# Optimization experiments

Hardware: AMD Instinct MI355X
Metric: run time of the kernel (lower is better)

The kernel has to match this reference:

```python
import jax, jax.numpy as jnp
import numpy as np

H = 16  # num heads


def setup_inputs() -> dict:
    key = jax.random.key(0)
    ks = jax.random.split(key, 12)
    B, S, D = 2, 2048, 1024
    f = lambda k, shape: jax.random.normal(k, shape, dtype=jnp.float32) * 0.02
    return {
        "Q": jax.random.normal(ks[0], (B, S, D), dtype=jnp.float32),
        "K": jax.random.normal(ks[1], (B, S, D), dtype=jnp.float32),
        "V": jax.random.normal(ks[2], (B, S, D), dtype=jnp.float32),
        "mask": jax.random.randint(ks[3], (B, S, S), 0, 2, dtype=jnp.int32),
        "Wq": f(ks[4], (D, D)), "bq": f(ks[5], (D,)),
        "Wk": f(ks[6], (D, D)), "bk": f(ks[7], (D,)),
        "Wv": f(ks[8], (D, D)), "bv": f(ks[9], (D,)),
        "Wo": f(ks[10], (D, D)), "bo": f(ks[11], (D,)),
    }


def mha(Q, K, V, mask, Wq, bq, Wk, bk, Wv, bv, Wo, bo):
    B, S, D = Q.shape
    d_k = D // H
    # torch Linear: x @ W.T + b
    q = (Q @ Wq.T + bq).reshape(B, S, H, d_k).transpose(0, 2, 1, 3)  # [B,H,S,dk]
    k = (K @ Wk.T + bk).reshape(B, S, H, d_k).transpose(0, 2, 1, 3)
    v = (V @ Wv.T + bv).reshape(B, S, H, d_k).transpose(0, 2, 1, 3)
    scores = jnp.einsum('bhqd,bhkd->bhqk', q, k) / jnp.sqrt(jnp.float32(d_k))
    # faithful to torch: mask.repeat(H,1,1) tiles batch-major along dim0 of [B*H,S,S]
    m = jnp.tile(mask, (H, 1, 1)).reshape(B, H, S, S)
    scores = jnp.where(m == 0, jnp.float32(-1e9), scores)
    attn = jax.nn.softmax(scores, axis=-1)                 # [B,H,S,S]
    ctx = jnp.einsum('bhqk,bhkd->bhqd', attn, v)           # [B,H,S,dk]
    ctx = ctx.transpose(0, 2, 1, 3).reshape(B, S, D)
    out = ctx @ Wo.T + bo
    return out, attn


def reference(Q, K, V, mask, Wq, bq, Wk, bk, Wv, bv, Wo, bo):
    return mha(Q, K, V, mask, Wq, bq, Wk, bk, Wv, bv, Wo, bo)
```

## Files before the change

kernel.cpp:

```cpp
#include <hip/hip_runtime.h>
#include <stdint.h>


typedef __attribute__((ext_vector_type(8))) short bf16x8;
typedef __attribute__((ext_vector_type(4))) float f32x4;
typedef unsigned long long u64;

#define MFMA16(a, b, c) __builtin_amdgcn_mfma_f32_16x16x32_bf16((a), (b), (c), 0, 0, 0)

#define GLDS16(g, l)                                                   \
  __builtin_amdgcn_global_load_lds(                                    \
      (const __attribute__((address_space(1))) unsigned int*)(g),      \
      (__attribute__((address_space(3))) unsigned int*)(l), 16, 0, 0)

__device__ __forceinline__ float bf2f(short s) {
  union { float f; unsigned u; } x;
  x.u = ((unsigned)(unsigned short)s) << 16;
  return x.f;
}
__device__ __forceinline__ short f2bf(float f) {
  union { float f; unsigned u; } x;
  x.f = f;
  unsigned r = x.u + 0x7fffu + ((x.u >> 16) & 1u);
  return (short)(r >> 16);
}
__device__ __forceinline__ unsigned cvtpk2(float lo, float hi) {
  unsigned r;
  asm("v_cvt_pk_bf16_f32 %0, %1, %2" : "=v"(r) : "v"(lo), "v"(hi));
  return r;
}
__device__ __forceinline__ bf16x8 pack8(float4 a, float4 b) {
  union { unsigned u[4]; bf16x8 v; } x;
  x.u[0] = cvtpk2(a.x, a.y);
  x.u[1] = cvtpk2(a.z, a.w);
  x.u[2] = cvtpk2(b.x, b.y);
  x.u[3] = cvtpk2(b.z, b.w);
  return x.v;
}

__global__ __launch_bounds__(256) void sentinel_fill(float* __restrict__ out,
                                                     float v, int n) {
  int i = blockIdx.x * 256 + threadIdx.x;
  if (i < n) out[i] = v;
}

__global__ __launch_bounds__(256) void pack_mask(const int* __restrict__ m,
                                                 u64* __restrict__ p) {
  long idx = (long)blockIdx.x * 256 + threadIdx.x;
  u64 b = __ballot(m[idx] != 0);
  if ((threadIdx.x & 63) == 0) p[idx >> 6] = b;
}

struct QkvPtrs {
  const float *A0, *A1, *A2;
  const float *W0, *W1, *W2;
  const float *c0, *c1, *c2;
  short *o0, *o1, *o2;
};
__global__ __launch_bounds__(256) void gemm_qkv(QkvPtrs p) {
  __shared__ short As[128 * 32];
  __shared__ short Bs[128 * 32];
  const int z = blockIdx.z;
  const float* Af = z == 0 ? p.A0 : (z == 1 ? p.A1 : p.A2);
  const float* W = z == 0 ? p.W0 : (z == 1 ? p.W1 : p.W2);
  const float* bias = z == 0 ? p.c0 : (z == 1 ? p.c1 : p.c2);
  short* outs = z == 0 ? p.o0 : (z == 1 ? p.o1 : p.o2);

  const int tid = threadIdx.x;
  const int lane = tid & 63;
  const int wid = tid >> 6;
  const int wr = wid >> 1, wc = wid & 1;
  const int m0 = blockIdx.x * 128;
  const int n0 = blockIdx.y * 128;

  const int srow = tid >> 1;
  const int scol = (tid & 1) << 4;
  const long aoff = (long)(m0 + srow) * 1024 + scol;
  const float* Wg = W + (long)(n0 + srow) * 1024 + scol;
  short* sA = As + srow * 32 + scol;
  short* sB = Bs + srow * 32 + scol;

  f32x4 acc[4][4] = {};
  const int fr = lane & 15;
  const int fc = (lane >> 4) << 3;

  for (int k0 = 0; k0 < 1024; k0 += 32) {
    __syncthreads();
    float4 x0 = *(const float4*)(Af + aoff + k0);
    float4 x1 = *(const float4*)(Af + aoff + k0 + 4);
    float4 x2 = *(const float4*)(Af + aoff + k0 + 8);
    float4 x3 = *(const float4*)(Af + aoff + k0 + 12);
    float4 w0 = *(const float4*)(Wg + k0);
    float4 w1 = *(const float4*)(Wg + k0 + 4);
    float4 w2 = *(const float4*)(Wg + k0 + 8);
    float4 w3 = *(const float4*)(Wg + k0 + 12);
    *(bf16x8*)sA = pack8(x0, x1);
    *(bf16x8*)(sA + 8) = pack8(x2, x3);
    *(bf16x8*)sB = pack8(w0, w1);
    *(bf16x8*)(sB + 8) = pack8(w2, w3);
    __syncthreads();
    bf16x8 a[4], b[4];
#pragma unroll
    for (int i = 0; i < 4; ++i)
      a[i] = *(const bf16x8*)&As[(wr * 64 + i * 16 + fr) * 32 + fc];
#pragma unroll
    for (int i = 0; i < 4; ++i)
      b[i] = *(const bf16x8*)&Bs[(wc * 64 + i * 16 + fr) * 32 + fc];
#pragma unroll
    for (int i = 0; i < 4; ++i)
#pragma unroll
      for (int j = 0; j < 4; ++j)
        acc[i][j] = MFMA16(a[i], b[j], acc[i][j]);
  }

#pragma unroll
  for (int i = 0; i < 4; ++i) {
    const int row0 = m0 + wr * 64 + i * 16 + (lane >> 4) * 4;
#pragma unroll
    for (int j = 0; j < 4; ++j) {
      const int col = n0 + wc * 64 + j * 16 + fr;
      const float bv = bias[col];
      const int h = col >> 6, dd = col & 63;
      if (z != 2) {
#pragma unroll
        for (int r = 0; r < 4; ++r) {
          const int m = row0 + r;
          float val = acc[i][j][r] + bv;
          if (z == 0) val *= 0.125f;
          const long o = (((long)(m >> 11) * 16 + h) * 2048 + (m & 2047)) * 64 + dd;
          outs[o] = f2bf(val);
        }
      } else {
        const long o = (((long)(row0 >> 11) * 16 + h) * 64 + dd) * 2048 + (row0 & 2047);
        union { unsigned short us[4]; uint2 v; } pk;
#pragma unroll
        for (int r = 0; r < 4; ++r) pk.us[r] = (unsigned short)f2bf(acc[i][j][r] + bv);
        *(uint2*)&outs[o] = pk.v;
      }
    }
  }
}

__global__ __launch_bounds__(256) void gemm_out(const short* __restrict__ Ab,
                                                const float* __restrict__ W,
                                                const float* __restrict__ bias,
                                                float* __restrict__ outf) {
  __shared__ short As[128 * 32];
  __shared__ short Bs[128 * 32];
  const int tid = threadIdx.x;
  const int lane = tid & 63;
  const int wid = tid >> 6;
  const int wr = wid >> 1, wc = wid & 1;
  const int m0 = blockIdx.x * 128;
  const int n0 = blockIdx.y * 128;

  const int srow = tid >> 1;
  const int scol = (tid & 1) << 4;
  const long aoff = (long)(m0 + srow) * 1024 + scol;
  const float* Wg = W + (long)(n0 + srow) * 1024 + scol;
  short* sA = As + srow * 32 + scol;
  short* sB = Bs + srow * 32 + scol;

  f32x4 acc[4][4] = {};
  const int fr = lane & 15;
  const int fc = (lane >> 4) << 3;

  for (int k0 = 0; k0 < 1024; k0 += 32) {
    __syncthreads();
    bf16x8 va0 = *(const bf16x8*)(Ab + aoff + k0);
    bf16x8 va1 = *(const bf16x8*)(Ab + aoff + k0 + 8);
    float4 w0 = *(const float4*)(Wg + k0);
    float4 w1 = *(const float4*)(Wg + k0 + 4);
    float4 w2 = *(const float4*)(Wg + k0 + 8);
    float4 w3 = *(const float4*)(Wg + k0 + 12);
    *(bf16x8*)sA = va0;
    *(bf16x8*)(sA + 8) = va1;
    *(bf16x8*)sB = pack8(w0, w1);
    *(bf16x8*)(sB + 8) = pack8(w2, w3);
    __syncthreads();
    bf16x8 a[4], b[4];
#pragma unroll
    for (int i = 0; i < 4; ++i)
      a[i] = *(const bf16x8*)&As[(wr * 64 + i * 16 + fr) * 32 + fc];
#pragma unroll
    for (int i = 0; i < 4; ++i)
      b[i] = *(const bf16x8*)&Bs[(wc * 64 + i * 16 + fr) * 32 + fc];
#pragma unroll
    for (int i = 0; i < 4; ++i)
#pragma unroll
      for (int j = 0; j < 4; ++j)
        acc[i][j] = MFMA16(a[i], b[j], acc[i][j]);
  }

#pragma unroll
  for (int i = 0; i < 4; ++i) {
    const int row0 = m0 + wr * 64 + i * 16 + (lane >> 4) * 4;
#pragma unroll
    for (int j = 0; j < 4; ++j) {
      const int col = n0 + wc * 64 + j * 16 + fr;
      const float bv = bias[col];
#pragma unroll
      for (int r = 0; r < 4; ++r)
        outf[(long)(row0 + r) * 1024 + col] = acc[i][j][r] + bv;
    }
  }
}

__global__ __launch_bounds__(256) void attn_fused(
    const short* __restrict__ qw, const short* __restrict__ kw,
    const short* __restrict__ vtw, const u64* __restrict__ pm,
    float* __restrict__ attn, short* __restrict__ ctx) {
  __shared__ short Ks[2][4096];
  __shared__ short Vs[2][4096];
  __shared__ short P[4][1024];
  const int tid = threadIdx.x;
  const int lane = tid & 63;
  const int wid = tid >> 6;
  const int bh = blockIdx.x;
  const int mb = bh & 1;
  const int q0 = blockIdx.y * 64 + wid * 16;
  const int fr = lane & 15;
  const int fg = lane >> 4;
  short* Pw = P[wid];

  bf16x8 aq[2];
  {
    const short* qb = qw + ((long)bh * 2048 + q0 + fr) * 64 + fg * 8;
    aq[0] = *(const bf16x8*)qb;
    aq[1] = *(const bf16x8*)(qb + 32);
  }

  const u64* mbase = pm + ((long)mb * 2048 + q0) * 32;
  const short* kbase = kw + (long)bh * 2048 * 64;
  const short* vbase = vtw + (long)bh * 64 * 2048;
  const long arow = (long)bh * 2048 + q0;

  const int sidx0 = tid;
  const int sidx1 = 256 + tid;
  const int sr0 = sidx0 >> 3, ss0 = (sidx0 ^ sr0) & 7;
  const int sr1 = sidx1 >> 3, ss1 = (sidx1 ^ sr1) & 7;
  short* ldst0 = &Ks[0][0] + (long)(wid * 64) * 8;
  short* ldst1 = &Ks[0][0] + (long)(256 + wid * 64) * 8;
  const long kofs = (long)(&Vs[0][0] - &Ks[0][0]);

#define STAGE_K(buf, kt)                                              \
  {                                                                   \
    const short* s_ = kbase + (long)((kt) * 64) * 64;                 \
    GLDS16(s_ + sr0 * 64 + ss0 * 8, ldst0 + (buf) * 4096);            \
    GLDS16(s_ + sr1 * 64 + ss1 * 8, ldst1 + (buf) * 4096);            \
  }
#define STAGE_V(buf, kt)                                              \
  {                                                                   \
    const short* s_ = vbase + (kt) * 64;                              \
    GLDS16(s_ + (long)sr0 * 2048 + ss0 * 8, ldst0 + kofs + (buf) * 4096); \
    GLDS16(s_ + (long)sr1 * 2048 + ss1 * 8, ldst1 + kofs + (buf) * 4096); \
  }
#define SWZ(row, slot) (((row) << 6) + ((((slot) ^ ((row) & 7))) << 3))
#define PADDR(row, col) \
  (((row) << 6) + (((((col) >> 3) ^ ((row) & 7))) << 3) + ((col) & 7))
#define WRITEBACK(kt)                                                 \
  {                                                                   \
    _Pragma("unroll") for (int c = 0; c < 4; ++c) {                   \
      const int idx = c * 64 + lane;                                  \
      const int row = idx >> 4;                                       \
      const int col = (idx & 15) * 4;                                 \
      union { uint2 w; short s[4]; } v4;                              \
      v4.w = *(const uint2*)&Pw[PADDR(row, col)];                     \
      float4 f;                                                       \
      f.x = bf2f(v4.s[0]); f.y = bf2f(v4.s[1]);                       \
      f.z = bf2f(v4.s[2]); f.w = bf2f(v4.s[3]);                       \
      *(float4*)&attn[(arow + row) * 2048 + (kt) * 64 + col] = f;     \
    }                                                                 \
  }
#define WAITBAR(N)                                                    \
  {                                                                   \
    asm volatile("s_waitcnt vmcnt(" #N ")" ::: "memory");             \
    __builtin_amdgcn_sched_barrier(0);                                \
    __builtin_amdgcn_s_barrier();                                     \
    __builtin_amdgcn_sched_barrier(0);                                \
  }

  float rs = 0.f;
  STAGE_K(0, 0);
  u64 mrow = mbase[fr * 32 + 0];
  WAITBAR(1)
  int cur = 0;
  for (int kt = 0; kt < 32; ++kt) {
    u64 mrow_next = 0;
    if (kt < 31) {
      STAGE_K(cur ^ 1, kt + 1);
      mrow_next = mbase[fr * 32 + kt + 1];
    }
#pragma unroll
    for (int ni = 0; ni < 4; ++ni) {
      const int R = ni * 16 + fr;
      bf16x8 b0 = *(const bf16x8*)&Ks[cur][SWZ(R, fg)];
      bf16x8 b1 = *(const bf16x8*)&Ks[cur][SWZ(R, 4 + fg)];
      const int kb0 = ni * 16 + fg * 4;
      const unsigned m4 = (unsigned)(mrow >> kb0) & 0xFu;
      f32x4 s = {0.f, 0.f, 0.f, 0.f};
      s = MFMA16(b0, aq[0], s);
      s = MFMA16(b1, aq[1], s);
#pragma unroll
      for (int r = 0; r < 4; ++r)
        if ((m4 >> r) & 1u) rs += __expf(s[r]);
    }
    if (kt < 31) {
      WAITBAR(1)
      cur ^= 1;
      mrow = mrow_next;
    }
  }
  float il;
  {
    float v = rs;
    v += __shfl_xor(v, 16);
    v += __shfl_xor(v, 32);
    il = 1.0f / v;
  }
  __builtin_amdgcn_s_barrier();

  f32x4 cacc[4] = {};
  STAGE_K(0, 0);
  STAGE_V(0, 0);
  mrow = mbase[fr * 32 + 0];
  WAITBAR(1)
  cur = 0;
  for (int kt = 0; kt < 32; ++kt) {
    u64 mrow_next = 0;
    if (kt < 31) {
      STAGE_K(cur ^ 1, kt + 1);
      STAGE_V(cur ^ 1, kt + 1);
      mrow_next = mbase[fr * 32 + kt + 1];
    }

#pragma unroll
    for (int ni = 0; ni < 4; ++ni) {
      const int R = ni * 16 + fr;
      bf16x8 b0 = *(const bf16x8*)&Ks[cur][SWZ(R, fg)];
      bf16x8 b1 = *(const bf16x8*)&Ks[cur][SWZ(R, 4 + fg)];
      const int kb0 = ni * 16 + fg * 4;
      const unsigned m4 = (unsigned)(mrow >> kb0) & 0xFu;
      f32x4 s = {0.f, 0.f, 0.f, 0.f};
      s = MFMA16(b0, aq[0], s);
      s = MFMA16(b1, aq[1], s);
      float p0 = (m4 & 1u) ? __expf(s[0]) * il : 0.0f;
      float p1 = (m4 & 2u) ? __expf(s[1]) * il : 0.0f;
      float p2 = (m4 & 4u) ? __expf(s[2]) * il : 0.0f;
      float p3 = (m4 & 8u) ? __expf(s[3]) * il : 0.0f;
      uint2 pk;
      pk.x = cvtpk2(p0, p1);
      pk.y = cvtpk2(p2, p3);
      *(uint2*)&Pw[PADDR(fr, kb0)] = pk;
    }

#pragma unroll
    for (int ks = 0; ks < 2; ++ks) {
      bf16x8 pa = *(const bf16x8*)&Pw[PADDR(fr, ks * 32 + fg * 8)];
#pragma unroll
      for (int ni = 0; ni < 4; ++ni) {
        const int R = ni * 16 + fr;
        bf16x8 bv = *(const bf16x8*)&Vs[cur][SWZ(R, ks * 4 + fg)];
        cacc[ni] = MFMA16(pa, bv, cacc[ni]);
      }
    }

    WRITEBACK(kt);

    if (kt < 31) {
      WAITBAR(5)
      cur ^= 1;
      mrow = mrow_next;
    }
  }

  const int b_ = bh >> 4, h_ = bh & 15;
#pragma unroll
  for (int ni = 0; ni < 4; ++ni)
#pragma unroll
    for (int r = 0; r < 4; ++r)
      ctx[((long)b_ * 2048 + q0 + fg * 4 + r) * 1024 + h_ * 64 + ni * 16 + fr] =
          f2bf(cacc[ni][r]);
#undef STAGE_K
#undef STAGE_V
#undef SWZ
#undef PADDR
#undef WRITEBACK
#undef WAITBAR
}

extern "C" void kernel_launch(void* const* d_in, const int* in_sizes, int n_in,
                              void* d_out, int out_size, void* d_ws,
                              size_t ws_size, hipStream_t stream) {
  float* out_o = (float*)d_out;

  const bool sizes_ok =
      (n_in == 12) && in_sizes[0] == 4194304 && in_sizes[1] == 4194304 &&
      in_sizes[2] == 4194304 && in_sizes[3] == 8388608 &&
      in_sizes[4] == 1048576 && in_sizes[5] == 1024 &&
      in_sizes[10] == 1048576 && in_sizes[11] == 1024 &&
      out_size == (2 * 2048 * 1024 + 2 * 16 * 2048 * 2048);
  const size_t WS_NEED = 34603008;
  if (!sizes_ok) {
    sentinel_fill<<<dim3(16384), 256, 0, stream>>>(out_o, 555.0f, 4194304);
    return;
  }
  if (ws_size < WS_NEED) {
    sentinel_fill<<<dim3(16384), 256, 0, stream>>>(out_o, 777.0f, 4194304);
    return;
  }

  const float* Q = (const float*)d_in[0];
  const float* K = (const float*)d_in[1];
  const float* V = (const float*)d_in[2];
  const int* mask = (const int*)d_in[3];
  const float* Wq = (const float*)d_in[4];
  const float* bq = (const float*)d_in[5];
  const float* Wk = (const float*)d_in[6];
  const float* bk = (const float*)d_in[7];
  const float* Wv = (const float*)d_in[8];
  const float* bv = (const float*)d_in[9];
  const float* Wo = (const float*)d_in[10];
  const float* bo = (const float*)d_in[11];

  short* qws = (short*)d_ws;
  short* kws = qws + 4194304;
  short* vtws = kws + 4194304;
  short* ctxws = vtws + 4194304;
  u64* pmask = (u64*)(ctxws + 4194304);

  float* out_attn = out_o + 2 * 2048 * 1024;

  pack_mask<<<dim3(2 * 2048 * 2048 / 256), 256, 0, stream>>>(mask, pmask);
  QkvPtrs p = {Q, K, V, Wq, Wk, Wv, bq, bk, bv, qws, kws, vtws};
  gemm_qkv<<<dim3(32, 8, 3), 256, 0, stream>>>(p);
  attn_fused<<<dim3(32, 32), 256, 0, stream>>>(qws, kws, vtws, pmask,
                                               out_attn, ctxws);
  gemm_out<<<dim3(32, 8), 256, 0, stream>>>(ctxws, Wo, bo, out_o);
}
```

Baseline: 363.7 us.

## Fold log2e into Q scale and write attn directly from registers

Fold log2(e) into the Q scaling factor so softmax can use the raw v_exp_f32 (exp2) instruction instead of __expf. Write fp32 attention probabilities straight from registers instead of re-reading the bf16-packed P tile from LDS and widening it. This removes LDS reads and the bf16 round trip on the large attn output, and also makes attn more precise. The trade-off is store coalescing: each lane now writes 16-byte chunks per row, with rows spread across lanes.

```diff
diff --git a/kernel.cpp b/kernel.cpp
--- a/kernel.cpp
+++ b/kernel.cpp
@@ -27,6 +27,11 @@
 __device__ __forceinline__ unsigned cvtpk2(float lo, float hi) {
   unsigned r;
   asm("v_cvt_pk_bf16_f32 %0, %1, %2" : "=v"(r) : "v"(lo), "v"(hi));
+  return r;
+}
+__device__ __forceinline__ float fexp2(float x) {
+  float r;
+  asm("v_exp_f32 %0, %1" : "=v"(r) : "v"(x));
   return r;
 }
 __device__ __forceinline__ bf16x8 pack8(float4 a, float4 b) {
@@ -126,7 +131,7 @@
         for (int r = 0; r < 4; ++r) {
           const int m = row0 + r;
           float val = acc[i][j][r] + bv;
-          if (z == 0) val *= 0.125f;
+          if (z == 0) val *= 0.18033688011112042f;
           const long o = (((long)(m >> 11) * 16 + h) * 2048 + (m & 2047)) * 64 + dd;
           outs[o] = f2bf(val);
         }
@@ -258,20 +263,6 @@
 #define SWZ(row, slot) (((row) << 6) + ((((slot) ^ ((row) & 7))) << 3))
 #define PADDR(row, col) \
   (((row) << 6) + (((((col) >> 3) ^ ((row) & 7))) << 3) + ((col) & 7))
-#define WRITEBACK(kt)                                                 \
-  {                                                                   \
-    _Pragma("unroll") for (int c = 0; c < 4; ++c) {                   \
-      const int idx = c * 64 + lane;                                  \
-      const int row = idx >> 4;                                       \
-      const int col = (idx & 15) * 4;                                 \
-      union { uint2 w; short s[4]; } v4;                              \
-      v4.w = *(const uint2*)&Pw[PADDR(row, col)];                     \
-      float4 f;                                                       \
-      f.x = bf2f(v4.s[0]); f.y = bf2f(v4.s[1]);                       \
-      f.z = bf2f(v4.s[2]); f.w = bf2f(v4.s[3]);                       \
-      *(float4*)&attn[(arow + row) * 2048 + (kt) * 64 + col] = f;     \
-    }                                                                 \
-  }
 #define WAITBAR(N)                                                    \
   {                                                                   \
     asm volatile("s_waitcnt vmcnt(" #N ")" ::: "memory");             \
@@ -303,7 +294,7 @@
       s = MFMA16(b1, aq[1], s);
 #pragma unroll
       for (int r = 0; r < 4; ++r)
-        if ((m4 >> r) & 1u) rs += __expf(s[r]);
+        if ((m4 >> r) & 1u) rs += fexp2(s[r]);
     }
     if (kt < 31) {
       WAITBAR(1)
@@ -334,6 +325,7 @@
       mrow_next = mbase[fr * 32 + kt + 1];
     }
 
+    f32x4 pf0, pf1, pf2, pf3;
 #pragma unroll
     for (int ni = 0; ni < 4; ++ni) {
       const int R = ni * 16 + fr;
@@ -344,14 +336,19 @@
       f32x4 s = {0.f, 0.f, 0.f, 0.f};
       s = MFMA16(b0, aq[0], s);
       s = MFMA16(b1, aq[1], s);
-      float p0 = (m4 & 1u) ? __expf(s[0]) * il : 0.0f;
-      float p1 = (m4 & 2u) ? __expf(s[1]) * il : 0.0f;
-      float p2 = (m4 & 4u) ? __expf(s[2]) * il : 0.0f;
-      float p3 = (m4 & 8u) ? __expf(s[3]) * il : 0.0f;
+      f32x4 pf;
+      pf[0] = (m4 & 1u) ? fexp2(s[0]) * il : 0.0f;
+      pf[1] = (m4 & 2u) ? fexp2(s[1]) * il : 0.0f;
+      pf[2] = (m4 & 4u) ? fexp2(s[2]) * il : 0.0f;
+      pf[3] = (m4 & 8u) ? fexp2(s[3]) * il : 0.0f;
       uint2 pk;
-      pk.x = cvtpk2(p0, p1);
-      pk.y = cvtpk2(p2, p3);
+      pk.x = cvtpk2(pf[0], pf[1]);
+      pk.y = cvtpk2(pf[2], pf[3]);
       *(uint2*)&Pw[PADDR(fr, kb0)] = pk;
+      if (ni == 0) pf0 = pf;
+      else if (ni == 1) pf1 = pf;
+      else if (ni == 2) pf2 = pf;
+      else pf3 = pf;
     }
 
 #pragma unroll
@@ -365,7 +362,13 @@
       }
     }
 
-    WRITEBACK(kt);
+    {
+      float* arp = &attn[(arow + fr) * 2048 + kt * 64 + fg * 4];
+      *(f32x4*)(arp) = pf0;
+      *(f32x4*)(arp + 16) = pf1;
+      *(f32x4*)(arp + 32) = pf2;
+      *(f32x4*)(arp + 48) = pf3;
+    }
 
     if (kt < 31) {
       WAITBAR(5)
@@ -385,7 +388,6 @@
 #undef STAGE_V
 #undef SWZ
 #undef PADDR
-#undef WRITEBACK
 #undef WAITBAR
 }
 
```

Result: slower. 375.9 us (+3.4%).
